# Optimization experiments

Hardware: AMD Instinct MI355X
Metric: run time of the kernel (lower is better)

Reference implementation:

```python
import jax, jax.numpy as jnp
import numpy as np

QLEN, MLEN, BSZ, DMODEL, NHEAD, DHEAD, DFF = 1024, 1024, 4, 1024, 16, 64, 4096
KLEN = QLEN + MLEN


def _layernorm(x, g, b, eps=1e-5):
    mu = jnp.mean(x, axis=-1, keepdims=True)
    var = jnp.var(x, axis=-1, keepdims=True)
    return (x - mu) * jax.lax.rsqrt(var + eps) * g + b


def _rel_shift(x):
    # x: [qlen, klen, bsz, nhead] -- Transformer-XL shift trick
    q, k, b, n = x.shape
    x = jnp.pad(x, ((0, 0), (1, 0), (0, 0), (0, 0)))  # [q, k+1, b, n]
    x = x.reshape(k + 1, q, b, n)[1:]
    return x.reshape(q, k, b, n)


def setup_inputs() -> dict:
    key = jax.random.key(0)
    ks = jax.random.split(key, 16)
    s = 0.02
    inp = {
        "word_embed": jax.random.normal(ks[0], (QLEN, BSZ, DMODEL), jnp.float32),
        "pos_embed": jax.random.normal(ks[1], (KLEN, DMODEL), jnp.float32),
        "bias_q": jax.random.normal(ks[2], (NHEAD, DHEAD), jnp.float32) * s,
        "bias_k": jax.random.normal(ks[3], (NHEAD, DHEAD), jnp.float32) * s,
        "memories": jax.random.normal(ks[4], (MLEN, BSZ, DMODEL), jnp.float32),
        "W_qkv": jax.random.normal(ks[5], (DMODEL, 3 * NHEAD * DHEAD), jnp.float32) * s,
        "W_r": jax.random.normal(ks[6], (DMODEL, NHEAD * DHEAD), jnp.float32) * s,
        "W_o": jax.random.normal(ks[7], (NHEAD * DHEAD, DMODEL), jnp.float32) * s,
        "ln1_g": jnp.ones((DMODEL,), jnp.float32),
        "ln1_b": jnp.zeros((DMODEL,), jnp.float32),
        "W_ff1": jax.random.normal(ks[8], (DMODEL, DFF), jnp.float32) * s,
        "b_ff1": jnp.zeros((DFF,), jnp.float32),
        "W_ff2": jax.random.normal(ks[9], (DFF, DMODEL), jnp.float32) * s,
        "b_ff2": jnp.zeros((DMODEL,), jnp.float32),
        "ln2_g": jnp.ones((DMODEL,), jnp.float32),
        "ln2_b": jnp.zeros((DMODEL,), jnp.float32),
    }
    # causal mask with memory: position i may attend to j <= i + MLEN; True = masked
    i = jnp.arange(QLEN)[:, None]
    j = jnp.arange(KLEN)[None, :]
    inp["attention_mask"] = j > (i + MLEN)
    return inp


def reference(word_embed, pos_embed, bias_q, bias_k, attention_mask, memories,
              W_qkv, W_r, W_o, ln1_g, ln1_b, W_ff1, b_ff1, W_ff2, b_ff2, ln2_g, ln2_b):
    scale = 1.0 / np.sqrt(DHEAD)
    cat = jnp.concatenate([memories, word_embed], axis=0)  # [klen, b, d]
    w_heads = cat @ W_qkv  # [klen, b, 3*n*dh]
    q, k, v = jnp.split(w_heads, 3, axis=-1)
    q = q[-QLEN:].reshape(QLEN, BSZ, NHEAD, DHEAD)
    k = k.reshape(KLEN, BSZ, NHEAD, DHEAD)
    v = v.reshape(KLEN, BSZ, NHEAD, DHEAD)
    r = (pos_embed @ W_r).reshape(KLEN, NHEAD, DHEAD)

    AC = jnp.einsum('ibnd,jbnd->ijbn', q + bias_q, k)          # content term
    BD = jnp.einsum('ibnd,jnd->ijbn', q + bias_k, r)           # position term
    BD = _rel_shift(BD)
    score = (AC + BD) * scale
    score = jnp.where(attention_mask[:, :, None, None], -1e30, score)
    prob = jax.nn.softmax(score, axis=1)
    attn_vec = jnp.einsum('ijbn,jbnd->ibnd', prob, v).reshape(QLEN, BSZ, NHEAD * DHEAD)
    attn_out = attn_vec @ W_o
    out = _layernorm(word_embed + attn_out, ln1_g, ln1_b)       # post-LN (pre_lnorm=False)

    core = jax.nn.relu(out @ W_ff1 + b_ff1) @ W_ff2 + b_ff2
    return _layernorm(out + core, ln2_g, ln2_b)
```

## Files before the change

### kernel.cpp

```cpp
#include <hip/hip_runtime.h>


typedef __bf16 bf16x8 __attribute__((ext_vector_type(8)));
typedef float f32x4 __attribute__((ext_vector_type(4)));

#define DEVI __device__ __forceinline__

DEVI unsigned short f2bf(float f) {
  union { float f; unsigned int u; } v;
  v.f = f;
  unsigned int u = v.u;
  u += 0x7fffu + ((u >> 16) & 1u);
  return (unsigned short)(u >> 16);
}

DEVI void load16(const unsigned short* g, unsigned short* l) {
  __builtin_amdgcn_global_load_lds(
      (const __attribute__((address_space(1))) unsigned int*)g,
      (__attribute__((address_space(3))) unsigned int*)l, 16, 0, 0);
}

__global__ __launch_bounds__(256) void cvt_bf16_kernel(const float* __restrict__ in,
                                                       unsigned short* __restrict__ out) {
  const int i = blockIdx.x * 256 + threadIdx.x;
  float4 v = *(const float4*)(in + (size_t)i * 4);
  ushort4 o;
  o.x = f2bf(v.x);
  o.y = f2bf(v.y);
  o.z = f2bf(v.z);
  o.w = f2bf(v.w);
  *(ushort4*)(out + (size_t)i * 4) = o;
}

template <typename T>
__global__ __launch_bounds__(256) void transpose_to_bf16(
    const T* __restrict__ in, unsigned short* __restrict__ out, int R, int C) {
  __shared__ unsigned short t[64][72];
  const int tid = threadIdx.x;
  const size_t zoff = (size_t)blockIdx.z * R * C;
  const int r0 = blockIdx.y * 64, c0 = blockIdx.x * 64;
  const T* inp = in + zoff;
  unsigned short* outp = out + zoff;
#pragma unroll
  for (int it = 0; it < 4; ++it) {
    int f = tid + 256 * it;
    int r = f >> 4;
    int c4 = (f & 15) << 2;
    if constexpr (sizeof(T) == 4) {
      float4 v = *(const float4*)((const float*)inp + (size_t)(r0 + r) * C + c0 + c4);
      t[c4 + 0][r] = f2bf(v.x);
      t[c4 + 1][r] = f2bf(v.y);
      t[c4 + 2][r] = f2bf(v.z);
      t[c4 + 3][r] = f2bf(v.w);
    } else {
      ushort4 v = *(const ushort4*)((const unsigned short*)inp + (size_t)(r0 + r) * C + c0 + c4);
      t[c4 + 0][r] = v.x;
      t[c4 + 1][r] = v.y;
      t[c4 + 2][r] = v.z;
      t[c4 + 3][r] = v.w;
    }
  }
  __syncthreads();
#pragma unroll
  for (int it = 0; it < 4; ++it) {
    int f = tid + 256 * it;
    int cc = f >> 4;
    int r4 = (f & 15) << 2;
    ushort4 o;
    o.x = t[cc][r4 + 0];
    o.y = t[cc][r4 + 1];
    o.z = t[cc][r4 + 2];
    o.w = t[cc][r4 + 3];
    *(ushort4*)(outp + (size_t)(c0 + cc) * R + r0 + r4) = o;
  }
}

struct GemmArgs {
  const unsigned short* A;
  const unsigned short* Bt;
  int row_split;
  int M, N, K;
  const float* p0;
  const float* p1;
  const float* resid;
  float* outF;
  unsigned short* o0;
  unsigned short* o1;
  unsigned short* o2;
  unsigned short* o3;
  int relu;
};

constexpr int BM = 128, BK = 64;

template <int EPI, int WN = 4>
__global__ __launch_bounds__(256, 4) void gemm_kernel(GemmArgs ga) {
  constexpr int BN_ = WN * 32;
  __shared__ __align__(16) unsigned short As[BM * BK];
  __shared__ __align__(16) unsigned short Bs[BN_ * BK];

  int m0, n0;
  if constexpr (EPI == 0) {
    const int flat = blockIdx.x;
    int mt_, nt_;
    if (flat < 1024) {
      mt_ = flat >> 4;
      nt_ = 8 + (flat & 15);
    } else {
      const int f2 = flat - 1024;
      mt_ = 32 + (f2 >> 3);
      nt_ = f2 & 7;
    }
    m0 = mt_ * 128;
    n0 = nt_ * 128;
  } else {
    n0 = blockIdx.x * BN_;
    m0 = blockIdx.y * BM;
  }
  const int tid = threadIdx.x;
  const int lane = tid & 63;
  const int wv = tid >> 6;
  const int l15 = lane & 15;
  const int quad = lane >> 4;
  const int wm = wv & 1, wn = wv >> 1;
  const int K = ga.K;
  const int r8 = lane >> 3;
  const int sc = (lane & 7) ^ r8;

  const f32x4 fzero = {0.f, 0.f, 0.f, 0.f};
  f32x4 acc[4][WN];
#pragma unroll
  for (int i = 0; i < 4; ++i)
#pragma unroll
    for (int j = 0; j < WN; ++j) acc[i][j] = fzero;

  const unsigned short* Ab = ga.A + (size_t)(m0 + 32 * wv + r8) * K + sc * 8;
  const unsigned short* Bb = ga.Bt + (size_t)(n0 + (BN_ / 4) * wv + r8) * K + sc * 8;
  const int h7 = l15 & 7;

  for (int k0 = 0; k0 < K; k0 += BK) {
    __syncthreads();
#pragma unroll
    for (int it = 0; it < 4; ++it)
      load16(Ab + (size_t)(8 * it) * K + k0, &As[(32 * wv + 8 * it) * 64]);
#pragma unroll
    for (int it = 0; it < BN_ / 32; ++it)
      load16(Bb + (size_t)(8 * it) * K + k0, &Bs[((BN_ / 4) * wv + 8 * it) * 64]);
    __syncthreads();
#pragma unroll
    for (int ks = 0; ks < 2; ++ks) {
      bf16x8 af[4], bg[WN];
#pragma unroll
      for (int mt = 0; mt < 4; ++mt)
        af[mt] = *(const bf16x8*)&As[(wm * 64 + mt * 16 + l15) * 64 +
                                     (((ks * 4 + quad) ^ h7) * 8)];
#pragma unroll
      for (int nt = 0; nt < WN; ++nt)
        bg[nt] = *(const bf16x8*)&Bs[(wn * (WN * 16) + nt * 16 + l15) * 64 +
                                     (((ks * 4 + quad) ^ h7) * 8)];
#pragma unroll
      for (int mt = 0; mt < 4; ++mt)
#pragma unroll
        for (int nt = 0; nt < WN; ++nt)
          acc[mt][nt] =
              __builtin_amdgcn_mfma_f32_16x16x32_bf16(af[mt], bg[nt], acc[mt][nt], 0, 0, 0);
    }
  }

#pragma unroll
  for (int mt = 0; mt < 4; ++mt) {
#pragma unroll
    for (int nt = 0; nt < WN; ++nt) {
#pragma unroll
      for (int r = 0; r < 4; ++r) {
        const int row = m0 + wm * 64 + mt * 16 + quad * 4 + r;
        const int col = n0 + wn * (WN * 16) + nt * 16 + l15;
        float val = acc[mt][nt][r];
        if constexpr (EPI == 0) {
          const int seq = row >> 2, b = row & 3;
          if (col < 1024) {
            if (seq >= 1024) {
              const int nh = col >> 6, d = col & 63;
              const size_t o = ((size_t)((b * 16 + nh) * 1024 + (seq - 1024))) * 64 + d;
              ga.o0[o] = f2bf(val + ga.p0[col]);
              ga.o1[o] = f2bf(val + ga.p1[col]);
            }
          } else if (col < 2048) {
            const int c = col - 1024, nh = c >> 6, d = c & 63, bn = b * 16 + nh;
            const size_t o = (size_t)bn * 131072 +
                             (size_t)(((seq >> 4) * 2 + (d >> 5)) * 512) +
                             ((((d >> 3) & 3) * 16 + (seq & 15)) * 8) + (d & 7);
            ga.o2[o] = f2bf(val);
          } else {
            const int c = col - 2048, nh = c >> 6, d = c & 63, bn = b * 16 + nh;
            const size_t o = (size_t)bn * 131072 + (size_t)((seq >> 7) * 8192) +
                             ((((seq >> 5) & 3) * 4 + (d >> 4)) * 512) +
                             ((((seq >> 3) & 3) * 16 + (d & 15)) * 8) + (seq & 7);
            ga.o3[o] = f2bf(val);
          }
        } else if constexpr (EPI == 1) {
          const int nh = col >> 6, d = col & 63, t = row;
          const size_t o = (size_t)nh * 131072 +
                           (size_t)(((t >> 4) * 2 + (d >> 5)) * 512) +
                           ((((d >> 3) & 3) * 16 + (t & 15)) * 8) + (d & 7);
          ga.o0[o] = f2bf(val);
        } else {
          if (ga.p0) val += ga.p0[col];
          if (ga.resid) val += ga.resid[(size_t)row * ga.N + col];
          if (ga.relu) val = fmaxf(val, 0.f);
          if (ga.outF) ga.outF[(size_t)row * ga.N + col] = val;
          if (ga.o0) ga.o0[(size_t)row * ga.N + col] = f2bf(val);
        }
      }
    }
  }
}

constexpr int P_LD = 136;
constexpr float CEXP = 0.18033688f;

__global__ __launch_bounds__(256, 4) void attn_kernel(
    const unsigned short* __restrict__ QQ, const unsigned short* __restrict__ QK,
    const unsigned short* __restrict__ Kf, const unsigned short* __restrict__ Vf,
    const unsigned short* __restrict__ Rf, unsigned short* __restrict__ AVb) {
  __shared__ __align__(16) unsigned short p_s[4][16 * P_LD];

  const int tid = threadIdx.x;
  const int lane = tid & 63;
  const int wv = tid >> 6;
  const int l15 = lane & 15;
  const int quad = lane >> 4;
  const int bn = blockIdx.x;
  const int iw = (blockIdx.y * 4 + wv) * 16;
  const int nh = bn & 15;
  const int bb = bn >> 4;
  unsigned short* pw = &p_s[wv][0];

  const unsigned short* kf = Kf + (size_t)bn * 131072;
  const unsigned short* vf = Vf + (size_t)bn * 131072;
  const unsigned short* rf = Rf + (size_t)nh * 131072;

  const size_t qoff = (size_t)bn * (1024 * 64) + (size_t)(iw + l15) * 64;
  const bf16x8 qq0 = *(const bf16x8*)(QQ + qoff + quad * 8);
  const bf16x8 qq1 = *(const bf16x8*)(QQ + qoff + 32 + quad * 8);
  const bf16x8 qk0 = *(const bf16x8*)(QK + qoff + quad * 8);
  const bf16x8 qk1 = *(const bf16x8*)(QK + qoff + 32 + quad * 8);

  const f32x4 fzero = {0.f, 0.f, 0.f, 0.f};
  f32x4 o_acc[4];
#pragma unroll
  for (int i = 0; i < 4; ++i) o_acc[i] = fzero;
  float lsum[4] = {0.f, 0.f, 0.f, 0.f};

  const int lane8 = lane * 8;
  const int jmax = iw + 15 + 1024;
  for (int j0 = 0; j0 <= jmax; j0 += 128) {
    const int t16b = (j0 >> 4) + 63 - (iw >> 4);
    f32x4 bd[9];
#pragma unroll
    for (int ct = 0; ct < 9; ++ct) {
      int tg = t16b + ct;
      tg = (tg < 127) ? tg : 127;
      const unsigned short* rb = rf + (size_t)(tg * 1024) + lane8;
      bf16x8 b0 = *(const bf16x8*)rb;
      bf16x8 b1 = *(const bf16x8*)(rb + 512);
      f32x4 c = fzero;
      c = __builtin_amdgcn_mfma_f32_16x16x32_bf16(qk0, b0, c, 0, 0, 0);
      c = __builtin_amdgcn_mfma_f32_16x16x32_bf16(qk1, b1, c, 0, 0, 0);
      bd[ct] = c;
    }

    const int ntb = j0 >> 4;
    f32x4 sv[8];
#pragma unroll
    for (int nt = 0; nt < 8; ++nt) {
      const unsigned short* kb = kf + (size_t)((ntb + nt) * 1024) + lane8;
      bf16x8 b0 = *(const bf16x8*)kb;
      bf16x8 b1 = *(const bf16x8*)(kb + 512);
      f32x4 c = fzero;
      c = __builtin_amdgcn_mfma_f32_16x16x32_bf16(qq0, b0, c, 0, 0, 0);
      c = __builtin_amdgcn_mfma_f32_16x16x32_bf16(qq1, b1, c, 0, 0, 0);
      sv[nt] = c;
    }

#pragma unroll
    for (int r = 0; r < 4; ++r) {
      const int il = quad * 4 + r;
      const int u = l15 + 15 - il;
      const int srcl = (lane & 48) | (u & 15);
      float w[9];
#pragma unroll
      for (int ct = 0; ct < 9; ++ct) w[ct] = __shfl(bd[ct][r], srcl, 64);
      const int ig = iw + il;
#pragma unroll
      for (int nt = 0; nt < 8; ++nt) {
        const float bdv = (u & 16) ? w[nt + 1] : w[nt];
        const int jg = j0 + nt * 16 + l15;
        float p = exp2f((sv[nt][r] + bdv) * CEXP);
        p = (jg > ig + 1024) ? 0.f : p;
        lsum[r] += p;
        pw[il * P_LD + nt * 16 + l15] = f2bf(p);
      }
    }

    const unsigned short* vb = vf + (size_t)((j0 >> 7) * 8192) + lane8;
#pragma unroll
    for (int ks = 0; ks < 4; ++ks) {
      bf16x8 ap = *(const bf16x8*)&pw[l15 * P_LD + ks * 32 + quad * 8];
#pragma unroll
      for (int nto = 0; nto < 4; ++nto) {
        bf16x8 bv = *(const bf16x8*)(vb + (ks * 4 + nto) * 512);
        o_acc[nto] = __builtin_amdgcn_mfma_f32_16x16x32_bf16(ap, bv, o_acc[nto], 0, 0, 0);
      }
    }
  }

  float linv[4];
#pragma unroll
  for (int r = 0; r < 4; ++r) {
    float l = lsum[r];
    l += __shfl_xor(l, 1, 64);
    l += __shfl_xor(l, 2, 64);
    l += __shfl_xor(l, 4, 64);
    l += __shfl_xor(l, 8, 64);
    linv[r] = 1.f / l;
  }
#pragma unroll
  for (int nto = 0; nto < 4; ++nto) {
#pragma unroll
    for (int r = 0; r < 4; ++r) {
      const int ig = iw + quad * 4 + r;
      const int d = nto * 16 + l15;
      const float val = o_acc[nto][r] * linv[r];
      AVb[(size_t)(ig * 4 + bb) * 1024 + nh * 64 + d] = f2bf(val);
    }
  }
}

__global__ __launch_bounds__(256) void ln_kernel(const float* __restrict__ x,
                                                 const float* __restrict__ g,
                                                 const float* __restrict__ bta,
                                                 float* __restrict__ outF,
                                                 unsigned short* __restrict__ outB) {
  const int row = blockIdx.x;
  const int tid = threadIdx.x;
  const float* xr = x + (size_t)row * 1024;
  const float4 v = *(const float4*)(xr + tid * 4);
  float s = v.x + v.y + v.z + v.w;
  float ss = v.x * v.x + v.y * v.y + v.z * v.z + v.w * v.w;
#pragma unroll
  for (int off = 1; off < 64; off <<= 1) {
    s += __shfl_xor(s, off, 64);
    ss += __shfl_xor(ss, off, 64);
  }
  __shared__ float red[8];
  const int wv = tid >> 6;
  if ((tid & 63) == 0) {
    red[wv] = s;
    red[4 + wv] = ss;
  }
  __syncthreads();
  s = red[0] + red[1] + red[2] + red[3];
  ss = red[4] + red[5] + red[6] + red[7];
  const float mu = s * (1.f / 1024.f);
  const float var = ss * (1.f / 1024.f) - mu * mu;
  const float rs = rsqrtf(var + 1e-5f);
  const float vv[4] = {v.x, v.y, v.z, v.w};
#pragma unroll
  for (int u = 0; u < 4; ++u) {
    const int c = tid * 4 + u;
    const float y = (vv[u] - mu) * rs * g[c] + bta[c];
    if (outF) outF[(size_t)row * 1024 + c] = y;
    if (outB) outB[(size_t)row * 1024 + c] = f2bf(y);
  }
}

extern "C" void kernel_launch(void* const* d_in, const int* in_sizes, int n_in,
                              void* d_out, int out_size, void* d_ws, size_t ws_size,
                              hipStream_t stream) {
  (void)in_sizes; (void)n_in; (void)out_size; (void)ws_size;
  const float* word_embed = (const float*)d_in[0];
  const float* pos_embed = (const float*)d_in[1];
  const float* bias_q = (const float*)d_in[2];
  const float* bias_k = (const float*)d_in[3];
  const float* memories = (const float*)d_in[4];
  const float* W_qkv = (const float*)d_in[5];
  const float* W_r = (const float*)d_in[6];
  const float* W_o = (const float*)d_in[7];
  const float* ln1_g = (const float*)d_in[8];
  const float* ln1_b = (const float*)d_in[9];
  const float* W_ff1 = (const float*)d_in[10];
  const float* b_ff1 = (const float*)d_in[11];
  const float* W_ff2 = (const float*)d_in[12];
  const float* b_ff2 = (const float*)d_in[13];
  const float* ln2_g = (const float*)d_in[14];
  const float* ln2_b = (const float*)d_in[15];
  float* out = (float*)d_out;

  char* ws = (char*)d_ws;
  unsigned short* QQ = (unsigned short*)(ws + 0);
  unsigned short* QK = (unsigned short*)(ws + 8388608);
  unsigned short* Kf = (unsigned short*)(ws + 16777216);
  unsigned short* Vf = (unsigned short*)(ws + 50331648);
  unsigned short* Rf = (unsigned short*)(ws + 67108864);
  unsigned short* AVb = (unsigned short*)(ws + 71303168);
  float* X1 = (float*)(ws + 79691776);
  float* OUT1 = (float*)(ws + 96468992);
  unsigned short* OUT1b = (unsigned short*)(ws + 113246208);
  unsigned short* Wqkv_t = (unsigned short*)(ws + 121634816);
  unsigned short* Wr_t = (unsigned short*)(ws + 127926272);
  unsigned short* Wo_t = (unsigned short*)(ws + 130023424);
  unsigned short* Wff1_t = (unsigned short*)(ws + 132120576);
  unsigned short* Wff2_t = (unsigned short*)(ws + 140509184);
  unsigned short* Catb = (unsigned short*)(ws + 79691776);
  unsigned short* Posb = (unsigned short*)(ws + 96468992);
  unsigned short* H = (unsigned short*)(ws + 0);
  float* C2 = X1;

  const dim3 blk(256);

  cvt_bf16_kernel<<<4096, blk, 0, stream>>>(memories, Catb);
  cvt_bf16_kernel<<<4096, blk, 0, stream>>>(word_embed, Catb + (size_t)4096 * 1024);
  cvt_bf16_kernel<<<2048, blk, 0, stream>>>(pos_embed, Posb);

  transpose_to_bf16<float><<<dim3(48, 16, 1), blk, 0, stream>>>(W_qkv, Wqkv_t, 1024, 3072);
  transpose_to_bf16<float><<<dim3(16, 16, 1), blk, 0, stream>>>(W_r, Wr_t, 1024, 1024);
  transpose_to_bf16<float><<<dim3(16, 16, 1), blk, 0, stream>>>(W_o, Wo_t, 1024, 1024);
  transpose_to_bf16<float><<<dim3(64, 16, 1), blk, 0, stream>>>(W_ff1, Wff1_t, 1024, 4096);
  transpose_to_bf16<float><<<dim3(16, 64, 1), blk, 0, stream>>>(W_ff2, Wff2_t, 4096, 1024);

  {
    GemmArgs a{};
    a.A = Catb;
    a.Bt = Wqkv_t;
    a.M = 8192; a.N = 3072; a.K = 1024;
    a.p0 = bias_q; a.p1 = bias_k;
    a.o0 = QQ; a.o1 = QK; a.o2 = Kf; a.o3 = Vf;
    gemm_kernel<0><<<dim3(1280), blk, 0, stream>>>(a);
  }
  {
    GemmArgs a{};
    a.A = Posb;
    a.Bt = Wr_t;
    a.M = 2048; a.N = 1024; a.K = 1024;
    a.o0 = Rf;
    gemm_kernel<1, 2><<<dim3(16, 16), blk, 0, stream>>>(a);
  }

  attn_kernel<<<dim3(64, 16), blk, 0, stream>>>(QQ, QK, Kf, Vf, Rf, AVb);

  {
    GemmArgs a{};
    a.A = AVb;
    a.Bt = Wo_t;
    a.M = 4096; a.N = 1024; a.K = 1024;
    a.resid = word_embed;
    a.outF = X1;
    gemm_kernel<2, 2><<<dim3(16, 32), blk, 0, stream>>>(a);
  }
  ln_kernel<<<4096, blk, 0, stream>>>(X1, ln1_g, ln1_b, OUT1, OUT1b);

  {
    GemmArgs a{};
    a.A = OUT1b;
    a.Bt = Wff1_t;
    a.M = 4096; a.N = 4096; a.K = 1024;
    a.p0 = b_ff1;
    a.relu = 1;
    a.o0 = H;
    gemm_kernel<2><<<dim3(32, 32), blk, 0, stream>>>(a);
  }
  {
    GemmArgs a{};
    a.A = H;
    a.Bt = Wff2_t;
    a.M = 4096; a.N = 1024; a.K = 4096;
    a.p0 = b_ff2;
    a.resid = OUT1;
    a.outF = C2;
    gemm_kernel<2, 2><<<dim3(16, 32), blk, 0, stream>>>(a);
  }
  ln_kernel<<<4096, blk, 0, stream>>>(C2, ln2_g, ln2_b, out, nullptr);
}
```

Measured before the change: 653.5 us.

## Triple-buffer GEMM LDS loads with async prefetch and uniform 128x64 tiles

Replaces the single-buffered GEMM with a three-stage LDS pipeline. It prefetches two K-tiles ahead through global_load_lds and uses explicit vmcnt waits with one barrier per iteration, so memory latency overlaps with MFMA work. All GEMMs now use a 128x64 tile, which doubles the grid for the QKV and FF1 GEMMs, and launch bounds drop to 2 blocks per SM because LDS use is larger. The gain depends on hiding load latency. The cost is lower occupancy and more redundant A-tile loads for the wider GEMMs that previously used 128x128 tiles.

```diff
diff --git a/kernel.cpp b/kernel.cpp
--- a/kernel.cpp
+++ b/kernel.cpp
@@ -91,31 +91,68 @@
   int relu;
 };
 
-constexpr int BM = 128, BK = 64;
-
-template <int EPI, int WN = 4>
-__global__ __launch_bounds__(256, 4) void gemm_kernel(GemmArgs ga) {
-  constexpr int BN_ = WN * 32;
-  __shared__ __align__(16) unsigned short As[BM * BK];
-  __shared__ __align__(16) unsigned short Bs[BN_ * BK];
+template <int EPI>
+DEVI void epi_store(const GemmArgs& ga, int row, int col, float val) {
+  if constexpr (EPI == 0) {
+    const int seq = row >> 2, b = row & 3;
+    if (col < 1024) {
+      if (seq >= 1024) {
+        const int nh = col >> 6, d = col & 63;
+        const size_t o = ((size_t)((b * 16 + nh) * 1024 + (seq - 1024))) * 64 + d;
+        ga.o0[o] = f2bf(val + ga.p0[col]);
+        ga.o1[o] = f2bf(val + ga.p1[col]);
+      }
+    } else if (col < 2048) {
+      const int c = col - 1024, nh = c >> 6, d = c & 63, bn = b * 16 + nh;
+      const size_t o = (size_t)bn * 131072 +
+                       (size_t)(((seq >> 4) * 2 + (d >> 5)) * 512) +
+                       ((((d >> 3) & 3) * 16 + (seq & 15)) * 8) + (d & 7);
+      ga.o2[o] = f2bf(val);
+    } else {
+      const int c = col - 2048, nh = c >> 6, d = c & 63, bn = b * 16 + nh;
+      const size_t o = (size_t)bn * 131072 + (size_t)((seq >> 7) * 8192) +
+                       ((((seq >> 5) & 3) * 4 + (d >> 4)) * 512) +
+                       ((((seq >> 3) & 3) * 16 + (d & 15)) * 8) + (seq & 7);
+      ga.o3[o] = f2bf(val);
+    }
+  } else if constexpr (EPI == 1) {
+    const int nh = col >> 6, d = col & 63, t = row;
+    const size_t o = (size_t)nh * 131072 +
+                     (size_t)(((t >> 4) * 2 + (d >> 5)) * 512) +
+                     ((((d >> 3) & 3) * 16 + (t & 15)) * 8) + (d & 7);
+    ga.o0[o] = f2bf(val);
+  } else {
+    if (ga.p0) val += ga.p0[col];
+    if (ga.resid) val += ga.resid[(size_t)row * ga.N + col];
+    if (ga.relu) val = fmaxf(val, 0.f);
+    if (ga.outF) ga.outF[(size_t)row * ga.N + col] = val;
+    if (ga.o0) ga.o0[(size_t)row * ga.N + col] = f2bf(val);
+  }
+}
+
+template <int EPI>
+__global__ __launch_bounds__(256, 2) void gemm_pipe(GemmArgs ga) {
+  __shared__ __align__(16) unsigned short As[3][128 * 64];
+  __shared__ __align__(16) unsigned short Bs[3][64 * 64];
 
   int m0, n0;
   if constexpr (EPI == 0) {
     const int flat = blockIdx.x;
+    const int f128 = flat >> 1;
     int mt_, nt_;
-    if (flat < 1024) {
-      mt_ = flat >> 4;
-      nt_ = 8 + (flat & 15);
+    if (f128 < 1024) {
+      mt_ = f128 >> 4;
+      nt_ = 8 + (f128 & 15);
     } else {
-      const int f2 = flat - 1024;
+      const int f2 = f128 - 1024;
       mt_ = 32 + (f2 >> 3);
       nt_ = f2 & 7;
     }
     m0 = mt_ * 128;
-    n0 = nt_ * 128;
+    n0 = nt_ * 128 + (flat & 1) * 64;
   } else {
-    n0 = blockIdx.x * BN_;
-    m0 = blockIdx.y * BM;
+    n0 = blockIdx.x * 64;
+    m0 = blockIdx.y * 128;
   }
   const int tid = threadIdx.x;
   const int lane = tid & 63;
@@ -126,94 +163,75 @@
   const int K = ga.K;
   const int r8 = lane >> 3;
   const int sc = (lane & 7) ^ r8;
+  const int h7 = l15 & 7;
+
+  const unsigned short* Ab = ga.A + (size_t)(m0 + 32 * wv + r8) * K + sc * 8;
+  const unsigned short* Bb = ga.Bt + (size_t)(n0 + 16 * wv + r8) * K + sc * 8;
 
   const f32x4 fzero = {0.f, 0.f, 0.f, 0.f};
-  f32x4 acc[4][WN];
+  f32x4 acc[4][2];
 #pragma unroll
   for (int i = 0; i < 4; ++i)
 #pragma unroll
-    for (int j = 0; j < WN; ++j) acc[i][j] = fzero;
-
-  const unsigned short* Ab = ga.A + (size_t)(m0 + 32 * wv + r8) * K + sc * 8;
-  const unsigned short* Bb = ga.Bt + (size_t)(n0 + (BN_ / 4) * wv + r8) * K + sc * 8;
-  const int h7 = l15 & 7;
-
-  for (int k0 = 0; k0 < K; k0 += BK) {
-    __syncthreads();
+    for (int j = 0; j < 2; ++j) acc[i][j] = fzero;
+
+  auto stage = [&](int kt, int bi) {
+    const int k0 = kt * 64;
 #pragma unroll
     for (int it = 0; it < 4; ++it)
-      load16(Ab + (size_t)(8 * it) * K + k0, &As[(32 * wv + 8 * it) * 64]);
-#pragma unroll
-    for (int it = 0; it < BN_ / 32; ++it)
-      load16(Bb + (size_t)(8 * it) * K + k0, &Bs[((BN_ / 4) * wv + 8 * it) * 64]);
-    __syncthreads();
+      load16(Ab + (size_t)(8 * it) * K + k0, &As[bi][(32 * wv + 8 * it) * 64]);
+#pragma unroll
+    for (int it = 0; it < 2; ++it)
+      load16(Bb + (size_t)(8 * it) * K + k0, &Bs[bi][(16 * wv + 8 * it) * 64]);
+  };
+
+  const int NT = K >> 6;
+  stage(0, 0);
+  stage(1, 1);
+  asm volatile("s_waitcnt vmcnt(6)" ::: "memory");
+  __builtin_amdgcn_s_barrier();
+
+  int bi = 0;
+  int bsn = 2;
+  for (int t = 0; t < NT; ++t) {
+    if (t + 2 < NT) stage(t + 2, bsn);
 #pragma unroll
     for (int ks = 0; ks < 2; ++ks) {
-      bf16x8 af[4], bg[WN];
+      bf16x8 af[4], bg[2];
 #pragma unroll
       for (int mt = 0; mt < 4; ++mt)
-        af[mt] = *(const bf16x8*)&As[(wm * 64 + mt * 16 + l15) * 64 +
-                                     (((ks * 4 + quad) ^ h7) * 8)];
-#pragma unroll
-      for (int nt = 0; nt < WN; ++nt)
-        bg[nt] = *(const bf16x8*)&Bs[(wn * (WN * 16) + nt * 16 + l15) * 64 +
-                                     (((ks * 4 + quad) ^ h7) * 8)];
+        af[mt] = *(const bf16x8*)&As[bi][(wm * 64 + mt * 16 + l15) * 64 +
+                                        (((ks * 4 + quad) ^ h7) * 8)];
+#pragma unroll
+      for (int nt = 0; nt < 2; ++nt)
+        bg[nt] = *(const bf16x8*)&Bs[bi][(wn * 32 + nt * 16 + l15) * 64 +
+                                         (((ks * 4 + quad) ^ h7) * 8)];
 #pragma unroll
       for (int mt = 0; mt < 4; ++mt)
 #pragma unroll
-        for (int nt = 0; nt < WN; ++nt)
+        for (int nt = 0; nt < 2; ++nt)
           acc[mt][nt] =
               __builtin_amdgcn_mfma_f32_16x16x32_bf16(af[mt], bg[nt], acc[mt][nt], 0, 0, 0);
     }
-  }
-
-#pragma unroll
-  for (int mt = 0; mt < 4; ++mt) {
-#pragma unroll
-    for (int nt = 0; nt < WN; ++nt) {
+    if (t + 2 < NT)
+      asm volatile("s_waitcnt vmcnt(6)" ::: "memory");
+    else
+      asm volatile("s_waitcnt vmcnt(0)" ::: "memory");
+    __builtin_amdgcn_s_barrier();
+    bi = (bi == 2) ? 0 : bi + 1;
+    bsn = (bsn == 2) ? 0 : bsn + 1;
+  }
+
+#pragma unroll
+  for (int mt = 0; mt < 4; ++mt)
+#pragma unroll
+    for (int nt = 0; nt < 2; ++nt)
 #pragma unroll
       for (int r = 0; r < 4; ++r) {
         const int row = m0 + wm * 64 + mt * 16 + quad * 4 + r;
-        const int col = n0 + wn * (WN * 16) + nt * 16 + l15;
-        float val = acc[mt][nt][r];
-        if constexpr (EPI == 0) {
-          const int seq = row >> 2, b = row & 3;
-          if (col < 1024) {
-            if (seq >= 1024) {
-              const int nh = col >> 6, d = col & 63;
-              const size_t o = ((size_t)((b * 16 + nh) * 1024 + (seq - 1024))) * 64 + d;
-              ga.o0[o] = f2bf(val + ga.p0[col]);
-              ga.o1[o] = f2bf(val + ga.p1[col]);
-            }
-          } else if (col < 2048) {
-            const int c = col - 1024, nh = c >> 6, d = c & 63, bn = b * 16 + nh;
-            const size_t o = (size_t)bn * 131072 +
-                             (size_t)(((seq >> 4) * 2 + (d >> 5)) * 512) +
-                             ((((d >> 3) & 3) * 16 + (seq & 15)) * 8) + (d & 7);
-            ga.o2[o] = f2bf(val);
-          } else {
-            const int c = col - 2048, nh = c >> 6, d = c & 63, bn = b * 16 + nh;
-            const size_t o = (size_t)bn * 131072 + (size_t)((seq >> 7) * 8192) +
-                             ((((seq >> 5) & 3) * 4 + (d >> 4)) * 512) +
-                             ((((seq >> 3) & 3) * 16 + (d & 15)) * 8) + (seq & 7);
-            ga.o3[o] = f2bf(val);
-          }
-        } else if constexpr (EPI == 1) {
-          const int nh = col >> 6, d = col & 63, t = row;
-          const size_t o = (size_t)nh * 131072 +
-                           (size_t)(((t >> 4) * 2 + (d >> 5)) * 512) +
-                           ((((d >> 3) & 3) * 16 + (t & 15)) * 8) + (d & 7);
-          ga.o0[o] = f2bf(val);
-        } else {
-          if (ga.p0) val += ga.p0[col];
-          if (ga.resid) val += ga.resid[(size_t)row * ga.N + col];
-          if (ga.relu) val = fmaxf(val, 0.f);
-          if (ga.outF) ga.outF[(size_t)row * ga.N + col] = val;
-          if (ga.o0) ga.o0[(size_t)row * ga.N + col] = f2bf(val);
-        }
+        const int col = n0 + wn * 32 + nt * 16 + l15;
+        epi_store<EPI>(ga, row, col, acc[mt][nt][r]);
       }
-    }
-  }
 }
 
 constexpr int P_LD = 136;
@@ -436,7 +454,7 @@
     a.M = 8192; a.N = 3072; a.K = 1024;
     a.p0 = bias_q; a.p1 = bias_k;
     a.o0 = QQ; a.o1 = QK; a.o2 = Kf; a.o3 = Vf;
-    gemm_kernel<0><<<dim3(1280), blk, 0, stream>>>(a);
+    gemm_pipe<0><<<dim3(2560), blk, 0, stream>>>(a);
   }
   {
     GemmArgs a{};
@@ -444,7 +462,7 @@
     a.Bt = Wr_t;
     a.M = 2048; a.N = 1024; a.K = 1024;
     a.o0 = Rf;
-    gemm_kernel<1, 2><<<dim3(16, 16), blk, 0, stream>>>(a);
+    gemm_pipe<1><<<dim3(16, 16), blk, 0, stream>>>(a);
   }
 
   attn_kernel<<<dim3(64, 16), blk, 0, stream>>>(QQ, QK, Kf, Vf, Rf, AVb);
@@ -456,7 +474,7 @@
     a.M = 4096; a.N = 1024; a.K = 1024;
     a.resid = word_embed;
     a.outF = X1;
-    gemm_kernel<2, 2><<<dim3(16, 32), blk, 0, stream>>>(a);
+    gemm_pipe<2><<<dim3(16, 32), blk, 0, stream>>>(a);
   }
   ln_kernel<<<4096, blk, 0, stream>>>(X1, ln1_g, ln1_b, OUT1, OUT1b);
 
@@ -468,7 +486,7 @@
     a.p0 = b_ff1;
     a.relu = 1;
     a.o0 = H;
-    gemm_kernel<2><<<dim3(32, 32), blk, 0, stream>>>(a);
+    gemm_pipe<2><<<dim3(64, 32), blk, 0, stream>>>(a);
   }
   {
     GemmArgs a{};
@@ -478,7 +496,7 @@
     a.p0 = b_ff2;
     a.resid = OUT1;
     a.outF = C2;
-    gemm_kernel<2, 2><<<dim3(16, 32), blk, 0, stream>>>(a);
+    gemm_pipe<2><<<dim3(16, 32), blk, 0, stream>>>(a);
   }
   ln_kernel<<<4096, blk, 0, stream>>>(C2, ln2_g, ln2_b, out, nullptr);
 }
```

After: 681.3 us. 1.04x slower.

## Split-K the W_o and FF2 GEMMs and fuse the partial-sum reduction into layernorm

Applied to the files above, without the earlier changes.

The two N=1024 GEMMs (attention output projection and FF2) now launch with a z-dimension of 2, each half covering half of K and writing fp32 partial results to workspace. A new layernorm kernel sums the two partials, adds the bias and residual, then normalizes, replacing the GEMM epilogue. This doubles the block count of these small-grid GEMMs (512 to 1024 blocks) to fill the GPU better. In exchange it adds extra fp32 partial-buffer write and read traffic.

```diff
diff --git a/kernel.cpp b/kernel.cpp
--- a/kernel.cpp
+++ b/kernel.cpp
@@ -78,7 +78,7 @@
 struct GemmArgs {
   const unsigned short* A;
   const unsigned short* Bt;
-  int row_split;
+  int Ks;
   int M, N, K;
   const float* p0;
   const float* p1;
@@ -89,6 +89,7 @@
   unsigned short* o2;
   unsigned short* o3;
   int relu;
+  int partial;
 };
 
 constexpr int BM = 128, BK = 64;
@@ -117,6 +118,7 @@
     n0 = blockIdx.x * BN_;
     m0 = blockIdx.y * BM;
   }
+  const int bz = blockIdx.z;
   const int tid = threadIdx.x;
   const int lane = tid & 63;
   const int wv = tid >> 6;
@@ -124,6 +126,7 @@
   const int quad = lane >> 4;
   const int wm = wv & 1, wn = wv >> 1;
   const int K = ga.K;
+  const int Ks = ga.Ks;
   const int r8 = lane >> 3;
   const int sc = (lane & 7) ^ r8;
 
@@ -134,11 +137,13 @@
 #pragma unroll
     for (int j = 0; j < WN; ++j) acc[i][j] = fzero;
 
-  const unsigned short* Ab = ga.A + (size_t)(m0 + 32 * wv + r8) * K + sc * 8;
-  const unsigned short* Bb = ga.Bt + (size_t)(n0 + (BN_ / 4) * wv + r8) * K + sc * 8;
+  const unsigned short* Ab =
+      ga.A + (size_t)(m0 + 32 * wv + r8) * K + sc * 8 + (size_t)bz * Ks;
+  const unsigned short* Bb =
+      ga.Bt + (size_t)(n0 + (BN_ / 4) * wv + r8) * K + sc * 8 + (size_t)bz * Ks;
   const int h7 = l15 & 7;
 
-  for (int k0 = 0; k0 < K; k0 += BK) {
+  for (int k0 = 0; k0 < Ks; k0 += BK) {
     __syncthreads();
 #pragma unroll
     for (int it = 0; it < 4; ++it)
@@ -205,11 +210,15 @@
                            ((((d >> 3) & 3) * 16 + (t & 15)) * 8) + (d & 7);
           ga.o0[o] = f2bf(val);
         } else {
-          if (ga.p0) val += ga.p0[col];
-          if (ga.resid) val += ga.resid[(size_t)row * ga.N + col];
-          if (ga.relu) val = fmaxf(val, 0.f);
-          if (ga.outF) ga.outF[(size_t)row * ga.N + col] = val;
-          if (ga.o0) ga.o0[(size_t)row * ga.N + col] = f2bf(val);
+          if (ga.partial) {
+            ga.outF[(size_t)bz * ((size_t)ga.M * ga.N) + (size_t)row * ga.N + col] = val;
+          } else {
+            if (ga.p0) val += ga.p0[col];
+            if (ga.resid) val += ga.resid[(size_t)row * ga.N + col];
+            if (ga.relu) val = fmaxf(val, 0.f);
+            if (ga.outF) ga.outF[(size_t)row * ga.N + col] = val;
+            if (ga.o0) ga.o0[(size_t)row * ga.N + col] = f2bf(val);
+          }
         }
       }
     }
@@ -337,21 +346,31 @@
   }
 }
 
-__global__ __launch_bounds__(256) void ln_kernel(const float* __restrict__ x,
-                                                 const float* __restrict__ g,
-                                                 const float* __restrict__ bta,
-                                                 float* __restrict__ outF,
-                                                 unsigned short* __restrict__ outB) {
+__global__ __launch_bounds__(256) void ln_sum_kernel(
+    const float* __restrict__ x0, const float* __restrict__ x1,
+    const float* __restrict__ bias, const float* __restrict__ resid,
+    const float* __restrict__ g, const float* __restrict__ bta,
+    float* __restrict__ outF, unsigned short* __restrict__ outB) {
   const int row = blockIdx.x;
   const int tid = threadIdx.x;
-  const float* xr = x + (size_t)row * 1024;
-  const float4 v = *(const float4*)(xr + tid * 4);
+  const size_t off = (size_t)row * 1024 + tid * 4;
+  float4 v = *(const float4*)(x0 + off);
+  const float4 w = *(const float4*)(x1 + off);
+  v.x += w.x; v.y += w.y; v.z += w.z; v.w += w.w;
+  if (bias) {
+    const float4 b = *(const float4*)(bias + tid * 4);
+    v.x += b.x; v.y += b.y; v.z += b.z; v.w += b.w;
+  }
+  if (resid) {
+    const float4 rr = *(const float4*)(resid + off);
+    v.x += rr.x; v.y += rr.y; v.z += rr.z; v.w += rr.w;
+  }
   float s = v.x + v.y + v.z + v.w;
   float ss = v.x * v.x + v.y * v.y + v.z * v.z + v.w * v.w;
 #pragma unroll
-  for (int off = 1; off < 64; off <<= 1) {
-    s += __shfl_xor(s, off, 64);
-    ss += __shfl_xor(ss, off, 64);
+  for (int off2 = 1; off2 < 64; off2 <<= 1) {
+    s += __shfl_xor(s, off2, 64);
+    ss += __shfl_xor(ss, off2, 64);
   }
   __shared__ float red[8];
   const int wv = tid >> 6;
@@ -404,7 +423,6 @@
   unsigned short* Vf = (unsigned short*)(ws + 50331648);
   unsigned short* Rf = (unsigned short*)(ws + 67108864);
   unsigned short* AVb = (unsigned short*)(ws + 71303168);
-  float* X1 = (float*)(ws + 79691776);
   float* OUT1 = (float*)(ws + 96468992);
   unsigned short* OUT1b = (unsigned short*)(ws + 113246208);
   unsigned short* Wqkv_t = (unsigned short*)(ws + 121634816);
@@ -415,7 +433,8 @@
   unsigned short* Catb = (unsigned short*)(ws + 79691776);
   unsigned short* Posb = (unsigned short*)(ws + 96468992);
   unsigned short* H = (unsigned short*)(ws + 0);
-  float* C2 = X1;
+  float* Pwo = (float*)(ws + 33554432);
+  float* Pff = (float*)(ws + 50331648);
 
   const dim3 blk(256);
 
@@ -433,7 +452,7 @@
     GemmArgs a{};
     a.A = Catb;
     a.Bt = Wqkv_t;
-    a.M = 8192; a.N = 3072; a.K = 1024;
+    a.M = 8192; a.N = 3072; a.K = 1024; a.Ks = 1024;
     a.p0 = bias_q; a.p1 = bias_k;
     a.o0 = QQ; a.o1 = QK; a.o2 = Kf; a.o3 = Vf;
     gemm_kernel<0><<<dim3(1280), blk, 0, stream>>>(a);
@@ -442,7 +461,7 @@
     GemmArgs a{};
     a.A = Posb;
     a.Bt = Wr_t;
-    a.M = 2048; a.N = 1024; a.K = 1024;
+    a.M = 2048; a.N = 1024; a.K = 1024; a.Ks = 1024;
     a.o0 = Rf;
     gemm_kernel<1, 2><<<dim3(16, 16), blk, 0, stream>>>(a);
   }
@@ -453,18 +472,19 @@
     GemmArgs a{};
     a.A = AVb;
     a.Bt = Wo_t;
-    a.M = 4096; a.N = 1024; a.K = 1024;
-    a.resid = word_embed;
-    a.outF = X1;
-    gemm_kernel<2, 2><<<dim3(16, 32), blk, 0, stream>>>(a);
-  }
-  ln_kernel<<<4096, blk, 0, stream>>>(X1, ln1_g, ln1_b, OUT1, OUT1b);
+    a.M = 4096; a.N = 1024; a.K = 1024; a.Ks = 512;
+    a.outF = Pwo;
+    a.partial = 1;
+    gemm_kernel<2, 2><<<dim3(16, 32, 2), blk, 0, stream>>>(a);
+  }
+  ln_sum_kernel<<<4096, blk, 0, stream>>>(Pwo, Pwo + (size_t)4096 * 1024, nullptr,
+                                          word_embed, ln1_g, ln1_b, OUT1, OUT1b);
 
   {
     GemmArgs a{};
     a.A = OUT1b;
     a.Bt = Wff1_t;
-    a.M = 4096; a.N = 4096; a.K = 1024;
+    a.M = 4096; a.N = 4096; a.K = 1024; a.Ks = 1024;
     a.p0 = b_ff1;
     a.relu = 1;
     a.o0 = H;
@@ -474,11 +494,11 @@
     GemmArgs a{};
     a.A = H;
     a.Bt = Wff2_t;
-    a.M = 4096; a.N = 1024; a.K = 4096;
-    a.p0 = b_ff2;
-    a.resid = OUT1;
-    a.outF = C2;
-    gemm_kernel<2, 2><<<dim3(16, 32), blk, 0, stream>>>(a);
-  }
-  ln_kernel<<<4096, blk, 0, stream>>>(C2, ln2_g, ln2_b, out, nullptr);
-}
+    a.M = 4096; a.N = 1024; a.K = 4096; a.Ks = 2048;
+    a.outF = Pff;
+    a.partial = 1;
+    gemm_kernel<2, 2><<<dim3(16, 32, 2), blk, 0, stream>>>(a);
+  }
+  ln_sum_kernel<<<4096, blk, 0, stream>>>(Pff, Pff + (size_t)4096 * 1024, b_ff2,
+                                          OUT1, ln2_g, ln2_b, out, nullptr);
+}
```

After: 629.5 us. 3.7% less time.
